# Performance work log

Hardware: AMD Instinct MI355X
Metric: run time of the kernel (lower is better)

Reference implementation:

```python
import jax, jax.numpy as jnp
import numpy as np

NUM_TOKENS = 32000
N_EMBD = 2048
N_HEAD = 16
HEAD_SIZE = N_EMBD // N_HEAD
MAX_LEN = 2048
SEQ = 2048


def _make_pe(max_len, d_model):
    position = np.arange(max_len, dtype=np.float32)[:, None]
    emb_idx = np.arange(0, d_model, 2, dtype=np.float32)
    div_term = 1.0 / np.power(10000.0, emb_idx / d_model)
    pe = np.zeros((max_len, d_model), dtype=np.float32)
    pe[:, 0::2] = np.sin(position * div_term)
    pe[:, 1::2] = np.cos(position * div_term)
    return jnp.asarray(pe)


def setup_inputs() -> dict:
    key = jax.random.key(0)
    ks = jax.random.split(key, 8)
    s = 1.0 / np.sqrt(N_EMBD)
    return {
        "token_ids": jax.random.randint(ks[0], (SEQ,), 0, NUM_TOKENS, dtype=jnp.int32),
        "we": jax.random.normal(ks[1], (NUM_TOKENS, N_EMBD), dtype=jnp.float32),
        "pe": _make_pe(MAX_LEN, N_EMBD),
        "Wq": jax.random.normal(ks[2], (N_HEAD, N_EMBD, HEAD_SIZE), dtype=jnp.float32) * s,
        "Wk": jax.random.normal(ks[3], (N_HEAD, N_EMBD, HEAD_SIZE), dtype=jnp.float32) * s,
        "Wv": jax.random.normal(ks[4], (N_HEAD, N_EMBD, HEAD_SIZE), dtype=jnp.float32) * s,
        "proj_w": jax.random.normal(ks[5], (N_EMBD, N_EMBD), dtype=jnp.float32) * s,
        "proj_b": jnp.zeros((N_EMBD,), dtype=jnp.float32),
        "fc_w": jax.random.normal(ks[6], (N_EMBD, NUM_TOKENS), dtype=jnp.float32) * s,
        "fc_b": jnp.zeros((NUM_TOKENS,), dtype=jnp.float32),
    }


def reference(token_ids, we, pe, Wq, Wk, Wv, proj_w, proj_b, fc_w, fc_b):
    T = token_ids.shape[0]
    x = we[token_ids] + pe[:T]                      # [T, D]
    # per-head QKV, stacked over heads: [H, T, hs]
    q = jnp.einsum('td,hdk->htk', x, Wq)
    k = jnp.einsum('td,hdk->htk', x, Wk)
    v = jnp.einsum('td,hdk->htk', x, Wv)
    scale = 1.0 / jnp.sqrt(jnp.asarray(HEAD_SIZE, dtype=x.dtype))
    sims = jnp.einsum('htk,hsk->hts', q, k) * scale  # [H, T, T]
    causal = jnp.tril(jnp.ones((T, T), dtype=bool))  # mask==0 where NOT lower-tri
    sims = jnp.where(causal[None], sims, jnp.asarray(-1e9, dtype=x.dtype))
    attn = jax.nn.softmax(sims, axis=-1)
    heads = jnp.einsum('hts,hsk->htk', attn, v)      # [H, T, hs]
    cat = jnp.transpose(heads, (1, 0, 2)).reshape(T, N_HEAD * HEAD_SIZE)
    sa = cat @ proj_w + proj_b                       # dropout = identity (eval)
    resid = x + sa
    return resid @ fc_w + fc_b                       # [T, num_tokens]
```

## Files before the change

### kernel.cpp

```cpp
#include <hip/hip_runtime.h>

#define T_SEQ 2048
#define D_EMB 2048
#define NHEAD 16
#define HS    128
#define NVOC  32000

typedef __attribute__((ext_vector_type(8))) short bf16x8;
typedef __attribute__((ext_vector_type(4))) float f32x4;
typedef unsigned short bfu;

__device__ __forceinline__ f32x4 mfma16(bf16x8 a, bf16x8 b, f32x4 c) {
    return __builtin_amdgcn_mfma_f32_16x16x32_bf16(a, b, c, 0, 0, 0);
}

__device__ __forceinline__ bfu f2bu(float f) {
    unsigned int u = __float_as_uint(f);
    unsigned int r = (u + 0x7fffu + ((u >> 16) & 1u)) >> 16;
    return (bfu)r;
}
__device__ __forceinline__ float b2f(bfu r) {
    return __uint_as_float((unsigned int)r << 16);
}

__device__ __forceinline__ void async_copy16(void* lds, const void* g) {
    __builtin_amdgcn_global_load_lds(
        (const __attribute__((address_space(1))) unsigned int*)g,
        (__attribute__((address_space(3))) unsigned int*)lds, 16, 0, 0);
}

#define SB0 __builtin_amdgcn_sched_barrier(0)
#define BARRIER __builtin_amdgcn_s_barrier()
#define WAIT_VM8   asm volatile("s_waitcnt vmcnt(8)" ::: "memory")
#define WAIT_VM6   asm volatile("s_waitcnt vmcnt(6)" ::: "memory")
#define WAIT_VM4   asm volatile("s_waitcnt vmcnt(4)" ::: "memory")
#define WAIT_VM2   asm volatile("s_waitcnt vmcnt(2)" ::: "memory")
#define WAIT_VM0   asm volatile("s_waitcnt vmcnt(0)" ::: "memory")

__device__ __forceinline__ void job_t64(const float* __restrict__ in,
                                        bfu* __restrict__ out, int R, int C,
                                        float scale, int tx, int ty, char* lds) {
    float (*tile)[65] = (float(*)[65])lds;
    const int r0 = ty * 64, c0 = tx * 64;
    const int t = threadIdx.x;
#pragma unroll
    for (int it = 0; it < 4; ++it) {
        int fi = it * 256 + t;
        int row = fi >> 4, c4 = (fi & 15) * 4;
        float4 v = *(const float4*)(in + (size_t)(r0 + row) * C + c0 + c4);
        tile[row][c4]     = v.x; tile[row][c4 + 1] = v.y;
        tile[row][c4 + 2] = v.z; tile[row][c4 + 3] = v.w;
    }
    __syncthreads();
#pragma unroll
    for (int it = 0; it < 4; ++it) {
        int ci = it * 256 + t;
        int oc = ci >> 4, r4 = (ci & 15) * 4;
        ushort4 u;
        u.x = f2bu(tile[r4 + 0][oc] * scale);
        u.y = f2bu(tile[r4 + 1][oc] * scale);
        u.z = f2bu(tile[r4 + 2][oc] * scale);
        u.w = f2bu(tile[r4 + 3][oc] * scale);
        *(ushort4*)(out + (size_t)(c0 + oc) * R + r0 + r4) = u;
    }
}

__device__ __forceinline__ void job_fcw256(const float* __restrict__ in,
                                           bfu* __restrict__ out, int tx, int ty,
                                           char* lds) {
    const int r0 = ty * 256, c0 = tx * 64;
    const int t = threadIdx.x;
#pragma unroll
    for (int it = 0; it < 16; ++it) {
        int fi = it * 256 + t;
        int row = fi >> 4, c4 = (fi & 15) * 4;
        float4 v = *(const float4*)(in + (size_t)(r0 + row) * NVOC + c0 + c4);
        ushort4 u;
        u.x = f2bu(v.x); u.y = f2bu(v.y); u.z = f2bu(v.z); u.w = f2bu(v.w);
        *(ushort4*)(lds + row * 128 + ((c4 * 2) ^ (((row >> 3) & 7) << 4))) = u;
    }
    __syncthreads();
#pragma unroll
    for (int it = 0; it < 8; ++it) {
        int idx = it * 256 + t;
        int oc = idx >> 5, r8 = (idx & 31) * 8;
        bf16x8 v;
#pragma unroll
        for (int j = 0; j < 8; ++j) {
            int row = r8 + j;
            v[j] = (short)*(const bfu*)(lds + row * 128 +
                                        ((oc * 2) ^ (((row >> 3) & 7) << 4)));
        }
        *(bf16x8*)(out + (size_t)(c0 + oc) * D_EMB + r0 + r8) = v;
    }
}

__global__ __launch_bounds__(256)
void k_prep(const int* __restrict__ ids, const float* __restrict__ we,
            const float* __restrict__ pe, bfu* __restrict__ xb,
            const float* __restrict__ Wq, const float* __restrict__ Wk,
            const float* __restrict__ Wv, const float* __restrict__ projw,
            const float* __restrict__ fcw, bfu* __restrict__ WqT,
            bfu* __restrict__ WkT, bfu* __restrict__ WvT,
            bfu* __restrict__ projT, bfu* __restrict__ fcwT, float qscale) {
    __shared__ __align__(16) char lds[256 * 65 * 4];
    int b = blockIdx.x;
    if (b < 4000) {
        job_fcw256(fcw, fcwT, b % 500, b / 500, lds);
    } else if (b < 5024) {
        int bb = b - 4000;
        job_t64(projw, projT, D_EMB, D_EMB, 1.0f, bb & 31, bb >> 5, lds);
    } else if (b < 8096) {
        int bb = b - 5024;
        int which = bb >> 10;
        bb &= 1023;
        int z = bb >> 6, rem = bb & 63;
        size_t zo = (size_t)z * D_EMB * HS;
        const float* in = (which == 0) ? Wq : (which == 1) ? Wk : Wv;
        bfu* out = (which == 0) ? WqT : (which == 1) ? WkT : WvT;
        job_t64(in + zo, out + zo, D_EMB, HS, (which == 0) ? qscale : 1.0f,
                rem & 1, rem >> 1, lds);
    } else {
        int tt = b - 8096;
        const int row = ids[tt];
        const float4* wr = (const float4*)(we + (size_t)row * D_EMB);
        const float4* pr = (const float4*)(pe + (size_t)tt * D_EMB);
        bfu* xbr = xb + (size_t)tt * D_EMB;
        int i = threadIdx.x;
#pragma unroll
        for (int r = 0; r < 2; ++r, i += 256) {
            float4 a = wr[i], p = pr[i];
            ushort4 u;
            u.x = f2bu(a.x + p.x); u.y = f2bu(a.y + p.y);
            u.z = f2bu(a.z + p.z); u.w = f2bu(a.w + p.w);
            *(ushort4*)(xbr + i * 4) = u;
        }
    }
}

__global__ void k_transpose_bf(const bfu* __restrict__ in, bfu* __restrict__ out,
                               int stride, int Tout) {
    __shared__ bfu tile[64][72];
    const int r0 = blockIdx.x * 64;
    const int c0 = blockIdx.y * 64;
    const int t = threadIdx.x;
#pragma unroll
    for (int it = 0; it < 2; ++it) {
        int idx = it * 256 + t;
        int row = idx >> 3, c8 = (idx & 7) * 8;
        *(bf16x8*)&tile[row][c8] = *(const bf16x8*)(in + (size_t)(r0 + row) * stride + c0 + c8);
    }
    __syncthreads();
#pragma unroll
    for (int it = 0; it < 2; ++it) {
        int idx = it * 256 + t;
        int oc = idx >> 3, r8 = (idx & 7) * 8;
        bf16x8 v;
#pragma unroll
        for (int j = 0; j < 8; ++j) v[j] = (short)tile[r8 + j][oc];
        *(bf16x8*)(out + (size_t)(c0 + oc) * Tout + r0 + r8) = v;
    }
}

template <int EPI>
__global__ __launch_bounds__(256, 2)
void k_gemm_nt(const bfu* __restrict__ A, const bfu* __restrict__ Bt,
               bfu* __restrict__ Cv, const float* __restrict__ bias,
               const bfu* __restrict__ resb, int M, int N, int K) {
    __shared__ __align__(16) char smem[2 * 128 * 64 * 2];
    const int tid = threadIdx.x;
    const int w = tid >> 6, lane = tid & 63;
    const int wr = w >> 1, wc = w & 1;
    const int lr = lane & 15, lk = lane >> 4;
    const int sw = ((lk ^ (lr & 7)) << 4);
    const int mb = M >> 7;
    const int m0 = (blockIdx.x % mb) << 7;
    const int n0 = (blockIdx.x / mb) << 7;
    char* As = smem;
    char* Bs = smem + 16384;
    f32x4 acc[4][4];
#pragma unroll
    for (int i = 0; i < 4; ++i)
#pragma unroll
        for (int j = 0; j < 4; ++j) acc[i][j] = (f32x4){0.f, 0.f, 0.f, 0.f};

    const bfu* Ag = A + (size_t)m0 * K;
    const bfu* Bg = Bt + (size_t)n0 * K;

    for (int kk = 0; kk < K; kk += 64) {
        __syncthreads();
#pragma unroll
        for (int r = 0; r < 4; ++r) {
            int i = r * 256 + tid;
            int row = i >> 3, slot = (i & 7) ^ (row & 7);
            async_copy16(As + (r * 256 + w * 64) * 16,
                         Ag + (size_t)row * K + kk + slot * 8);
        }
#pragma unroll
        for (int r = 0; r < 4; ++r) {
            int i = r * 256 + tid;
            int row = i >> 3, slot = (i & 7) ^ (row & 7);
            async_copy16(Bs + (r * 256 + w * 64) * 16,
                         Bg + (size_t)row * K + kk + slot * 8);
        }
        __syncthreads();
#pragma unroll
        for (int kc = 0; kc < 2; ++kc) {
            const int so = kc ? (sw ^ 64) : sw;
            bf16x8 a[4], b[4];
#pragma unroll
            for (int mf = 0; mf < 4; ++mf)
                a[mf] = *(const bf16x8*)(As + (wr * 64 + mf * 16 + lr) * 128 + so);
#pragma unroll
            for (int nf = 0; nf < 4; ++nf)
                b[nf] = *(const bf16x8*)(Bs + (wc * 64 + nf * 16 + lr) * 128 + so);
#pragma unroll
            for (int mf = 0; mf < 4; ++mf)
#pragma unroll
                for (int nf = 0; nf < 4; ++nf)
                    acc[mf][nf] = mfma16(a[mf], b[nf], acc[mf][nf]);
        }
    }
#pragma unroll
    for (int nf = 0; nf < 4; ++nf) {
        int col = n0 + wc * 64 + nf * 16 + lr;
        float bv = (EPI >= 1) ? bias[col] : 0.0f;
#pragma unroll
        for (int mf = 0; mf < 4; ++mf) {
            int row0 = m0 + wr * 64 + mf * 16 + lk * 4;
            f32x4 v = acc[mf][nf];
#pragma unroll
            for (int j = 0; j < 4; ++j) {
                size_t idx = (size_t)(row0 + j) * N + col;
                float val = v[j] + bv;
                if (EPI == 1) val += b2f(resb[idx]);
                Cv[idx] = f2bu(val);
            }
        }
    }
}

__device__ __forceinline__ void stage_chunk(char* sm, const bfu* A_, const bfu* B_,
                                            int K, int tt, int kind, int w,
                                            int laneRow, int laneCol) {
    char* base = sm + (size_t)(tt & 1) * 65536 + ((kind >= 2) ? 32768 : 0);
    const bfu* G = (kind >= 2) ? B_ : A_;
#pragma unroll
    for (int r = 0; r < 2; ++r) {
        int p = w * 2 + r;
        int row0 = (kind < 2) ? ((kind & 1) * 64 + (p & 7) * 8 + (p >> 3) * 128)
                              : ((kind & 1) * 32 + (p & 3) * 8 + (p >> 2) * 64);
        const char* g = (const char*)G + ((size_t)(row0 + laneRow) * K + tt * 64) * 2 + laneCol;
        async_copy16(base + row0 * 128, g);
    }
}

template <int Q>
__device__ __forceinline__ void read_A(bf16x8 (&aA)[2][4][2], const char* bufA,
                                       int wm, int lr, int sw0) {
    const char* p = bufA + ((wm * 128 + Q * 64 + lr) * 128);
#pragma unroll
    for (int mf = 0; mf < 4; ++mf) {
        aA[Q][mf][0] = *(const bf16x8*)(p + mf * 2048 + sw0);
        aA[Q][mf][1] = *(const bf16x8*)(p + mf * 2048 + (sw0 ^ 64));
    }
}

template <int Q>
__device__ __forceinline__ void read_B(bf16x8 (&bB)[2][2], const char* bufB,
                                       int wn, int lr, int sw0) {
    const char* p = bufB + ((wn * 64 + Q * 32 + lr) * 128);
#pragma unroll
    for (int nf = 0; nf < 2; ++nf) {
        bB[nf][0] = *(const bf16x8*)(p + nf * 2048 + sw0);
        bB[nf][1] = *(const bf16x8*)(p + nf * 2048 + (sw0 ^ 64));
    }
}

template <int QM, int QN>
__device__ __forceinline__ void mfma_quad(f32x4 (&acc)[8][4], bf16x8 (&aA)[2][4][2],
                                          bf16x8 (&bB)[2][2]) {
    __builtin_amdgcn_s_setprio(1);
#pragma unroll
    for (int kc = 0; kc < 2; ++kc)
#pragma unroll
        for (int mf = 0; mf < 4; ++mf)
#pragma unroll
            for (int nf = 0; nf < 2; ++nf)
                acc[QM * 4 + mf][QN * 2 + nf] =
                    mfma16(aA[QM][mf][kc], bB[nf][kc], acc[QM * 4 + mf][QN * 2 + nf]);
    __builtin_amdgcn_s_setprio(0);
}

template <int EPI>
__global__ __launch_bounds__(512, 2)
void k_gemm256(const bfu* __restrict__ A, const bfu* __restrict__ Bt,
               void* __restrict__ Cv, const float* __restrict__ bias,
               int M, int N, int K) {
    __shared__ __align__(16) char smem[2 * 65536];
    const int tid = threadIdx.x;
    const int w = tid >> 6, lane = tid & 63;
    const int wm = w >> 2, wn = w & 3;
    const int lr = lane & 15, lk = lane >> 4;
    const int sw0 = ((lk ^ (lr & 7)) << 4);
    const int laneRow = lane >> 3;
    const int laneCol = ((lane & 7) ^ (lane >> 3)) << 4;

    const int mb = M >> 8;
    const int nwgs = mb * (N >> 8);
    int bid = blockIdx.x;
    int swz = ((nwgs & 7) == 0) ? ((bid & 7) * (nwgs >> 3) + (bid >> 3)) : bid;
    const int m0 = (swz % mb) << 8;
    const int n0 = (swz / mb) << 8;

    const bfu* Ag = A + (size_t)m0 * K;
    const bfu* Bg = Bt + (size_t)n0 * K;

    f32x4 acc[8][4];
#pragma unroll
    for (int i = 0; i < 8; ++i)
#pragma unroll
        for (int j = 0; j < 4; ++j) acc[i][j] = (f32x4){0.f, 0.f, 0.f, 0.f};
    bf16x8 aA[2][4][2], bB[2][2];

    const int nkt = K >> 6;

    stage_chunk(smem, Ag, Bg, K, 0, 0, w, laneRow, laneCol);
    stage_chunk(smem, Ag, Bg, K, 0, 2, w, laneRow, laneCol);
    stage_chunk(smem, Ag, Bg, K, 0, 1, w, laneRow, laneCol);
    stage_chunk(smem, Ag, Bg, K, 0, 3, w, laneRow, laneCol);
    stage_chunk(smem, Ag, Bg, K, 1, 2, w, laneRow, laneCol);
    stage_chunk(smem, Ag, Bg, K, 1, 0, w, laneRow, laneCol);
    WAIT_VM8; SB0; BARRIER;

    for (int t = 0; t < nkt - 2; ++t) {
        const char* bufA = smem + (size_t)(t & 1) * 65536;
        const char* bufB = bufA + 32768;
        read_A<0>(aA, bufA, wm, lr, sw0);
        read_B<0>(bB, bufB, wn, lr, sw0);
        stage_chunk(smem, Ag, Bg, K, t + 1, 1, w, laneRow, laneCol);
        mfma_quad<0, 0>(acc, aA, bB);
        WAIT_VM8; BARRIER;

        read_A<1>(aA, bufA, wm, lr, sw0);
        stage_chunk(smem, Ag, Bg, K, t + 1, 3, w, laneRow, laneCol);
        mfma_quad<1, 0>(acc, aA, bB);
        WAIT_VM8; BARRIER;

        read_B<1>(bB, bufB, wn, lr, sw0);
        stage_chunk(smem, Ag, Bg, K, t + 2, 2, w, laneRow, laneCol);
        mfma_quad<0, 1>(acc, aA, bB);
        WAIT_VM8; BARRIER;

        stage_chunk(smem, Ag, Bg, K, t + 2, 0, w, laneRow, laneCol);
        mfma_quad<1, 1>(acc, aA, bB);
        WAIT_VM8; BARRIER;
    }

    {
        const int t = nkt - 2;
        const char* bufA = smem + (size_t)(t & 1) * 65536;
        const char* bufB = bufA + 32768;
        read_A<0>(aA, bufA, wm, lr, sw0);
        read_B<0>(bB, bufB, wn, lr, sw0);
        stage_chunk(smem, Ag, Bg, K, t + 1, 1, w, laneRow, laneCol);
        mfma_quad<0, 0>(acc, aA, bB);
        WAIT_VM8; BARRIER;

        read_A<1>(aA, bufA, wm, lr, sw0);
        stage_chunk(smem, Ag, Bg, K, t + 1, 3, w, laneRow, laneCol);
        mfma_quad<1, 0>(acc, aA, bB);
        WAIT_VM8; BARRIER;

        read_B<1>(bB, bufB, wn, lr, sw0);
        mfma_quad<0, 1>(acc, aA, bB);
        WAIT_VM6; BARRIER;

        mfma_quad<1, 1>(acc, aA, bB);
        WAIT_VM4; BARRIER;
    }
    {
        const int t = nkt - 1;
        const char* bufA = smem + (size_t)(t & 1) * 65536;
        const char* bufB = bufA + 32768;
        read_A<0>(aA, bufA, wm, lr, sw0);
        read_B<0>(bB, bufB, wn, lr, sw0);
        mfma_quad<0, 0>(acc, aA, bB);
        WAIT_VM2; BARRIER;

        read_A<1>(aA, bufA, wm, lr, sw0);
        mfma_quad<1, 0>(acc, aA, bB);
        WAIT_VM0; BARRIER;

        read_B<1>(bB, bufB, wn, lr, sw0);
        mfma_quad<0, 1>(acc, aA, bB);
        mfma_quad<1, 1>(acc, aA, bB);
    }

#pragma unroll
    for (int nfg = 0; nfg < 4; ++nfg) {
        int col = n0 + wn * 64 + nfg * 16 + lr;
        float bv = (EPI == 2) ? bias[col] : 0.0f;
#pragma unroll
        for (int mfg = 0; mfg < 8; ++mfg) {
            int row0 = m0 + wm * 128 + mfg * 16 + lk * 4;
            f32x4 v = acc[mfg][nfg];
#pragma unroll
            for (int j = 0; j < 4; ++j) {
                size_t idx = (size_t)(row0 + j) * N + col;
                if (EPI == 2) ((float*)Cv)[idx] = v[j] + bv;
                else          ((bfu*)Cv)[idx] = f2bu(v[j]);
            }
        }
    }
}

__global__ __launch_bounds__(256, 2)
void k_attn(const bfu* __restrict__ q, const bfu* __restrict__ k,
            const bfu* __restrict__ vT, bfu* __restrict__ o, int qks) {
    __shared__ __align__(16) char kvlds[2][32768];
    __shared__ __align__(16) bfu plds[4][16][72];
    const int w = threadIdx.x >> 6, lane = threadIdx.x & 63;
    const int lr = lane & 15, lk = lane >> 4;
    const int h = blockIdx.y;
    const int bxr = (gridDim.x - 1) - blockIdx.x;
    const int qrow = bxr * 64 + w * 16;
    const int sw = ((lk ^ (lr & 7)) << 4);

    const int krow = lane >> 4, kslot = lane & 15;
    const int vrow = lane >> 3, vslot = lane & 7;

    bf16x8 aq[4];
#pragma unroll
    for (int kc = 0; kc < 4; ++kc)
        aq[kc] = *(const bf16x8*)(q + (size_t)(qrow + lr) * qks + h * HS + kc * 32 + lk * 8);

    f32x4 O[8];
#pragma unroll
    for (int hf = 0; hf < 8; ++hf) O[hf] = (f32x4){0.f, 0.f, 0.f, 0.f};
    float m_[4], l_[4];
#pragma unroll
    for (int j = 0; j < 4; ++j) { m_[j] = -__builtin_inff(); l_[j] = 0.f; }

    const int nst = bxr + 1;

#define STAGE_KV(st)                                                            \
    {                                                                           \
        char* bK = kvlds[(st) & 1];                                             \
        char* bV = bK + 16384;                                                  \
        const int s0_ = (st) * 64;                                              \
        _Pragma("unroll")                                                       \
        for (int j = 0; j < 4; ++j) {                                           \
            int ir = w * 4 + j;                                                 \
            int krw = ir * 4 + krow;                                            \
            int kss = (kslot & 8) | ((kslot & 7) ^ (krw & 7));                  \
            async_copy16(bK + ir * 1024,                                        \
                         k + (size_t)(s0_ + krw) * qks + h * HS + kss * 8);     \
            int vrw = ir * 8 + vrow;                                            \
            int vss = vslot ^ (vrw & 7);                                        \
            async_copy16(bV + ir * 1024,                                        \
                         vT + (size_t)(h * HS + vrw) * T_SEQ + s0_ + vss * 8);  \
        }                                                                       \
    }

    STAGE_KV(0);
    WAIT_VM0; BARRIER;

    for (int st = 0; st < nst; ++st) {
        const char* bK = kvlds[st & 1];
        const char* bV = bK + 16384;
        const int s0 = st * 64;
        if (st + 1 < nst) STAGE_KV(st + 1);

        f32x4 S[4];
#pragma unroll
        for (int nf = 0; nf < 4; ++nf) S[nf] = (f32x4){0.f, 0.f, 0.f, 0.f};
#pragma unroll
        for (int nf = 0; nf < 4; ++nf) {
            const char* kp = bK + (nf * 16 + lr) * 256;
#pragma unroll
            for (int kc = 0; kc < 4; ++kc) {
                bf16x8 bk = *(const bf16x8*)(kp + ((kc & 2) << 6) + (sw ^ ((kc & 1) << 6)));
                S[nf] = mfma16(aq[kc], bk, S[nf]);
            }
        }
        if (s0 + 63 > qrow) {
#pragma unroll
            for (int nf = 0; nf < 4; ++nf) {
                int scol = s0 + nf * 16 + lr;
#pragma unroll
                for (int j = 0; j < 4; ++j)
                    if (scol > qrow + lk * 4 + j) S[nf][j] = -1e30f;
            }
        }
        float tm[4];
#pragma unroll
        for (int j = 0; j < 4; ++j)
            tm[j] = fmaxf(fmaxf(S[0][j], S[1][j]), fmaxf(S[2][j], S[3][j]));
#pragma unroll
        for (int d = 1; d < 16; d <<= 1)
#pragma unroll
            for (int j = 0; j < 4; ++j) tm[j] = fmaxf(tm[j], __shfl_xor(tm[j], d));
        float mn[4], ts[4];
#pragma unroll
        for (int j = 0; j < 4; ++j) mn[j] = fmaxf(m_[j], tm[j]);
#pragma unroll
        for (int nf = 0; nf < 4; ++nf)
#pragma unroll
            for (int j = 0; j < 4; ++j) S[nf][j] = __expf(S[nf][j] - mn[j]);
#pragma unroll
        for (int j = 0; j < 4; ++j) ts[j] = S[0][j] + S[1][j] + S[2][j] + S[3][j];
#pragma unroll
        for (int d = 1; d < 16; d <<= 1)
#pragma unroll
            for (int j = 0; j < 4; ++j) ts[j] += __shfl_xor(ts[j], d);
#pragma unroll
        for (int nf = 0; nf < 4; ++nf)
#pragma unroll
            for (int j = 0; j < 4; ++j)
                plds[w][lk * 4 + j][nf * 16 + lr] = f2bu(S[nf][j]);
#pragma unroll
        for (int j = 0; j < 4; ++j) {
            float f = __expf(m_[j] - mn[j]);
            l_[j] = l_[j] * f + ts[j];
            m_[j] = mn[j];
#pragma unroll
            for (int hf = 0; hf < 8; ++hf) O[hf][j] *= f;
        }
        bf16x8 pa[2];
#pragma unroll
        for (int kc2 = 0; kc2 < 2; ++kc2)
            pa[kc2] = *(const bf16x8*)(&plds[w][lr][kc2 * 32 + lk * 8]);
#pragma unroll
        for (int hf = 0; hf < 8; ++hf) {
            const char* vp = bV + (hf * 16 + lr) * 128;
#pragma unroll
            for (int kc2 = 0; kc2 < 2; ++kc2) {
                bf16x8 bv = *(const bf16x8*)(vp + (sw ^ (kc2 << 6)));
                O[hf] = mfma16(pa[kc2], bv, O[hf]);
            }
        }
        WAIT_VM0; BARRIER;
    }
#undef STAGE_KV

#pragma unroll
    for (int j = 0; j < 4; ++j) {
        float inv = 1.0f / l_[j];
        size_t rbase = (size_t)(qrow + lk * 4 + j) * D_EMB + h * HS;
#pragma unroll
        for (int hf = 0; hf < 8; ++hf)
            o[rbase + hf * 16 + lr] = f2bu(O[hf][j] * inv);
    }
}

extern "C" void kernel_launch(void* const* d_in, const int* in_sizes, int n_in,
                              void* d_out, int out_size, void* d_ws, size_t ws_size,
                              hipStream_t stream) {
    const int*   ids   = (const int*)d_in[0];
    const float* we    = (const float*)d_in[1];
    const float* pe    = (const float*)d_in[2];
    const float* Wq    = (const float*)d_in[3];
    const float* Wk    = (const float*)d_in[4];
    const float* Wv    = (const float*)d_in[5];
    const float* projw = (const float*)d_in[6];
    const float* projb = (const float*)d_in[7];
    const float* fcw   = (const float*)d_in[8];
    const float* fcb   = (const float*)d_in[9];
    float* out = (float*)d_out;
    (void)in_sizes; (void)n_in; (void)out_size; (void)ws_size;

    char* ws = (char*)d_ws;
    size_t off = 0;
    bfu*   fcwT  = (bfu*)(ws + off);  off += (size_t)NVOC * D_EMB * 2;
    bfu*   xb    = (bfu*)(ws + off);  off += (size_t)T_SEQ * D_EMB * 2;
    bfu*   qkvb  = (bfu*)(ws + off);  off += (size_t)T_SEQ * 3 * D_EMB * 2;
    bfu*   vTb   = (bfu*)(ws + off);  off += (size_t)D_EMB * T_SEQ * 2;
    bfu*   WqT   = (bfu*)(ws + off);  off += (size_t)D_EMB * D_EMB * 2;
    bfu*   WkT   = (bfu*)(ws + off);  off += (size_t)D_EMB * D_EMB * 2;
    bfu*   WvT   = (bfu*)(ws + off);  off += (size_t)D_EMB * D_EMB * 2;
    bfu*   projT = (bfu*)(ws + off);  off += (size_t)D_EMB * D_EMB * 2;
    bfu*   attnb = WqT;
    bfu*   resb  = WvT;

    const float qscale = 0.08838834764831845f;

    k_prep<<<10144, 256, 0, stream>>>(ids, we, pe, xb, Wq, Wk, Wv, projw, fcw,
                                      WqT, WkT, WvT, projT, fcwT, qscale);

    k_gemm256<0><<<(T_SEQ / 256) * (3 * D_EMB / 256), 512, 0, stream>>>(
        xb, WqT, qkvb, nullptr, T_SEQ, 3 * D_EMB, D_EMB);

    k_transpose_bf<<<dim3(T_SEQ / 64, D_EMB / 64), 256, 0, stream>>>(
        qkvb + 2 * D_EMB, vTb, 3 * D_EMB, T_SEQ);

    k_attn<<<dim3(T_SEQ / 64, NHEAD), 256, 0, stream>>>(qkvb, qkvb + D_EMB, vTb, attnb, 3 * D_EMB);

    k_gemm_nt<1><<<(T_SEQ / 128) * (D_EMB / 128), 256, 0, stream>>>(
        attnb, projT, resb, projb, xb, T_SEQ, D_EMB, D_EMB);

    k_gemm256<2><<<(T_SEQ / 256) * (NVOC / 256), 512, 0, stream>>>(
        resb, fcwT, out, fcb, T_SEQ, NVOC, D_EMB);
}
```

Baseline: 564.0 us.

## Move fc_w transpose-convert into QKV GEMM launch as trailing blocks

Moves the fc_w fp32-to-bf16 transpose jobs out of the prep kernel and appends them as extra workgroups after the QKV GEMM tiles in the same launch. The GEMM only has 192 tiles and does not fill the GPU, so the memory-bound conversion blocks can run alongside it on otherwise idle CUs. The prep kernel shrinks and uses less LDS. The cost is that the GEMM kernel now carries a branch and a second code path, and the conversion blocks may compete with the GEMM for memory bandwidth.

Measured after the change: 568.0 us. No clear change (+0.7%).

```diff
diff --git a/kernel.cpp b/kernel.cpp
--- a/kernel.cpp
+++ b/kernel.cpp
@@ -65,53 +65,19 @@
     }
 }
 
-__device__ __forceinline__ void job_fcw256(const float* __restrict__ in,
-                                           bfu* __restrict__ out, int tx, int ty,
-                                           char* lds) {
-    const int r0 = ty * 256, c0 = tx * 64;
-    const int t = threadIdx.x;
-#pragma unroll
-    for (int it = 0; it < 16; ++it) {
-        int fi = it * 256 + t;
-        int row = fi >> 4, c4 = (fi & 15) * 4;
-        float4 v = *(const float4*)(in + (size_t)(r0 + row) * NVOC + c0 + c4);
-        ushort4 u;
-        u.x = f2bu(v.x); u.y = f2bu(v.y); u.z = f2bu(v.z); u.w = f2bu(v.w);
-        *(ushort4*)(lds + row * 128 + ((c4 * 2) ^ (((row >> 3) & 7) << 4))) = u;
-    }
-    __syncthreads();
-#pragma unroll
-    for (int it = 0; it < 8; ++it) {
-        int idx = it * 256 + t;
-        int oc = idx >> 5, r8 = (idx & 31) * 8;
-        bf16x8 v;
-#pragma unroll
-        for (int j = 0; j < 8; ++j) {
-            int row = r8 + j;
-            v[j] = (short)*(const bfu*)(lds + row * 128 +
-                                        ((oc * 2) ^ (((row >> 3) & 7) << 4)));
-        }
-        *(bf16x8*)(out + (size_t)(c0 + oc) * D_EMB + r0 + r8) = v;
-    }
-}
-
 __global__ __launch_bounds__(256)
 void k_prep(const int* __restrict__ ids, const float* __restrict__ we,
             const float* __restrict__ pe, bfu* __restrict__ xb,
             const float* __restrict__ Wq, const float* __restrict__ Wk,
             const float* __restrict__ Wv, const float* __restrict__ projw,
-            const float* __restrict__ fcw, bfu* __restrict__ WqT,
-            bfu* __restrict__ WkT, bfu* __restrict__ WvT,
-            bfu* __restrict__ projT, bfu* __restrict__ fcwT, float qscale) {
-    __shared__ __align__(16) char lds[256 * 65 * 4];
+            bfu* __restrict__ WqT, bfu* __restrict__ WkT, bfu* __restrict__ WvT,
+            bfu* __restrict__ projT, float qscale) {
+    __shared__ __align__(16) char lds[64 * 65 * 4];
     int b = blockIdx.x;
-    if (b < 4000) {
-        job_fcw256(fcw, fcwT, b % 500, b / 500, lds);
-    } else if (b < 5024) {
-        int bb = b - 4000;
-        job_t64(projw, projT, D_EMB, D_EMB, 1.0f, bb & 31, bb >> 5, lds);
-    } else if (b < 8096) {
-        int bb = b - 5024;
+    if (b < 1024) {
+        job_t64(projw, projT, D_EMB, D_EMB, 1.0f, b & 31, b >> 5, lds);
+    } else if (b < 4096) {
+        int bb = b - 1024;
         int which = bb >> 10;
         bb &= 1023;
         int z = bb >> 6, rem = bb & 63;
@@ -121,7 +87,7 @@
         job_t64(in + zo, out + zo, D_EMB, HS, (which == 0) ? qscale : 1.0f,
                 rem & 1, rem >> 1, lds);
     } else {
-        int tt = b - 8096;
+        int tt = b - 4096;
         const int row = ids[tt];
         const float4* wr = (const float4*)(we + (size_t)row * D_EMB);
         const float4* pr = (const float4*)(pe + (size_t)tt * D_EMB);
@@ -292,12 +258,49 @@
     __builtin_amdgcn_s_setprio(0);
 }
 
-template <int EPI>
+__device__ __forceinline__ void job_fcw512(const float* __restrict__ in,
+                                           bfu* __restrict__ out, int tx, int ty,
+                                           char* lds) {
+    const int r0 = ty * 256, c0 = tx * 64;
+    const int t = threadIdx.x;
+#pragma unroll
+    for (int it = 0; it < 8; ++it) {
+        int fi = it * 512 + t;
+        int row = fi >> 4, c4 = (fi & 15) * 4;
+        float4 v = *(const float4*)(in + (size_t)(r0 + row) * NVOC + c0 + c4);
+        ushort4 u;
+        u.x = f2bu(v.x); u.y = f2bu(v.y); u.z = f2bu(v.z); u.w = f2bu(v.w);
+        *(ushort4*)(lds + row * 128 + ((c4 * 2) ^ (((row >> 3) & 7) << 4))) = u;
+    }
+    __syncthreads();
+#pragma unroll
+    for (int it = 0; it < 4; ++it) {
+        int idx = it * 512 + t;
+        int oc = idx >> 5, r8 = (idx & 31) * 8;
+        bf16x8 v;
+#pragma unroll
+        for (int j = 0; j < 8; ++j) {
+            int row = r8 + j;
+            v[j] = (short)*(const bfu*)(lds + row * 128 +
+                                        ((oc * 2) ^ (((row >> 3) & 7) << 4)));
+        }
+        *(bf16x8*)(out + (size_t)(c0 + oc) * D_EMB + r0 + r8) = v;
+    }
+}
+
+template <int EPI, bool FUSE_FCW>
 __global__ __launch_bounds__(512, 2)
 void k_gemm256(const bfu* __restrict__ A, const bfu* __restrict__ Bt,
                void* __restrict__ Cv, const float* __restrict__ bias,
-               int M, int N, int K) {
+               int M, int N, int K,
+               const float* __restrict__ fcw, bfu* __restrict__ fcwT,
+               int gemm_nwgs) {
     __shared__ __align__(16) char smem[2 * 65536];
+    if (FUSE_FCW && (int)blockIdx.x >= gemm_nwgs) {
+        int fb = blockIdx.x - gemm_nwgs;
+        job_fcw512(fcw, fcwT, fb % 500, fb / 500, smem);
+        return;
+    }
     const int tid = threadIdx.x;
     const int w = tid >> 6, lane = tid & 63;
     const int wm = w >> 2, wn = w & 3;
@@ -585,11 +588,11 @@
 
     const float qscale = 0.08838834764831845f;
 
-    k_prep<<<10144, 256, 0, stream>>>(ids, we, pe, xb, Wq, Wk, Wv, projw, fcw,
-                                      WqT, WkT, WvT, projT, fcwT, qscale);
-
-    k_gemm256<0><<<(T_SEQ / 256) * (3 * D_EMB / 256), 512, 0, stream>>>(
-        xb, WqT, qkvb, nullptr, T_SEQ, 3 * D_EMB, D_EMB);
+    k_prep<<<6144, 256, 0, stream>>>(ids, we, pe, xb, Wq, Wk, Wv, projw,
+                                     WqT, WkT, WvT, projT, qscale);
+
+    k_gemm256<0, true><<<192 + 4000, 512, 0, stream>>>(
+        xb, WqT, qkvb, nullptr, T_SEQ, 3 * D_EMB, D_EMB, fcw, fcwT, 192);
 
     k_transpose_bf<<<dim3(T_SEQ / 64, D_EMB / 64), 256, 0, stream>>>(
         qkvb + 2 * D_EMB, vTb, 3 * D_EMB, T_SEQ);
@@ -599,6 +602,6 @@
     k_gemm_nt<1><<<(T_SEQ / 128) * (D_EMB / 128), 256, 0, stream>>>(
         attnb, projT, resb, projb, xb, T_SEQ, D_EMB, D_EMB);
 
-    k_gemm256<2><<<(T_SEQ / 256) * (NVOC / 256), 512, 0, stream>>>(
-        resb, fcwT, out, fcb, T_SEQ, NVOC, D_EMB);
-}
+    k_gemm256<2, false><<<(T_SEQ / 256) * (NVOC / 256), 512, 0, stream>>>(
+        resb, fcwT, out, fcb, T_SEQ, NVOC, D_EMB, nullptr, nullptr, 0);
+}
```
